# Kernel tuning notes

Measured on AMD Instinct MI355X. Metric: run time of the kernel, lower is better.

## Reference

```python
import jax, jax.numpy as jnp
import numpy as np

# near_sym_a (5,7)-tap biorthogonal analysis filters used by DTCWT level 1
_H0O = np.array([-0.05, 0.25, 0.5, 0.25, -0.05], dtype=np.float32)
_H1O = np.array([-0.0107143, 0.0535714, 0.2607143, -0.6071429,
                 0.2607143, 0.0535714, -0.0107143], dtype=np.float32)

MAGBIAS = np.float32(0.01)


def _filt(x, h, axis):
    """Depthwise 1D correlation of NCHW x along `axis` (2=H rows, 3=W cols)
    with symmetric (half-sample reflect) padding; output same spatial size
    (odd-length filters)."""
    m = h.shape[0] // 2
    pad = [(0, 0)] * 4
    pad[axis] = (m, m)
    xp = jnp.pad(x, pad, mode='symmetric')
    n, c, hh, ww = xp.shape
    k = h.reshape(1, 1, -1, 1) if axis == 2 else h.reshape(1, 1, 1, -1)
    y = jax.lax.conv_general_dilated(
        xp.reshape(n * c, 1, hh, ww), k, (1, 1), 'VALID',
        dimension_numbers=('NCHW', 'OIHW', 'NCHW'))
    return y.reshape(n, c, y.shape[2], y.shape[3])


def _q2c(y):
    # quads -> two complex subimages: ((a-d) + j(b+c), (a+d) + j(b-c)) / sqrt(2)
    y = y * np.float32(1.0 / np.sqrt(2.0))
    a = y[..., 0::2, 0::2]
    b = y[..., 0::2, 1::2]
    c = y[..., 1::2, 0::2]
    d = y[..., 1::2, 1::2]
    return (a - d, b + c), (a + d, b - c)


def _scat_j1(x, h0o, h1o, magbias):
    # level-1 DTCWT: separable biorthogonal filtering (no decimation)
    lo = _filt(x, h0o, 3)   # row lowpass  (along W)
    hi = _filt(x, h1o, 3)   # row highpass
    ll = _filt(lo, h0o, 2)  # (N,C,H,W) lowpass
    lh = _filt(lo, h1o, 2)
    hl = _filt(hi, h0o, 2)
    hh = _filt(hi, h1o, 2)
    # quads -> 6 oriented complex subbands at half resolution
    (d15r, d15i), (d165r, d165i) = _q2c(lh)
    (d45r, d45i), (d135r, d135i) = _q2c(hh)
    (d75r, d75i), (d105r, d105i) = _q2c(hl)
    reals = jnp.stack([d15r, d45r, d75r, d105r, d135r, d165r], axis=1)  # (N,6,C,H/2,W/2)
    imags = jnp.stack([d15i, d45i, d75i, d105i, d135i, d165i], axis=1)
    # smoothed complex magnitude nonlinearity
    r = jnp.sqrt(reals * reals + imags * imags + magbias * magbias) - magbias
    # 2x2 average pool of lowpass
    n, c, hh_, ww_ = ll.shape
    ll = ll.reshape(n, c, hh_ // 2, 2, ww_ // 2, 2).mean(axis=(3, 5))
    b_, _, c_, h_, w_ = r.shape
    r = r.reshape(b_, 6 * c_, h_, w_)
    return ll, r


def setup_inputs() -> dict:
    key = jax.random.key(0)
    x = jax.random.normal(key, (32, 64, 128, 128), dtype=jnp.float32)
    # non-trainable wavelet filter "parameters" (fixed near_sym_a taps)
    return {"x": x, "h0o": jnp.asarray(_H0O), "h1o": jnp.asarray(_H1O)}


def reference(x, h0o, h1o):
    # H, W are even here so the odd-size edge-replication branch is a no-op
    return _scat_j1(x, h0o, h1o, MAGBIAS)
```

## Files before the change

### kernel.cpp

```cpp
#include <hip/hip_runtime.h>
#include <math.h>

#define HALO 3
#define TILE_IN 16
#define LROWS (TILE_IN + 2*HALO)
#define W 128
#define TILE_OUT 8
#define NTILES 8

__device__ __forceinline__ int refl128(int i) {
    i = (i < 0) ? (-1 - i) : i;
    return (i > 127) ? (255 - i) : i;
}

__device__ __forceinline__ float2 vdot7(const float2* A) {
    float2 r;
    r.x = fmaf(-0.0107143f, A[0].x + A[6].x,
          fmaf( 0.0535714f, A[1].x + A[5].x,
          fmaf( 0.2607143f, A[2].x + A[4].x, -0.6071429f * A[3].x)));
    r.y = fmaf(-0.0107143f, A[0].y + A[6].y,
          fmaf( 0.0535714f, A[1].y + A[5].y,
          fmaf( 0.2607143f, A[2].y + A[4].y, -0.6071429f * A[3].y)));
    return r;
}

__device__ __forceinline__ float2 vdot5(const float2* A) {
    float2 r;
    r.x = fmaf(-0.05f, A[0].x + A[4].x, fmaf(0.25f, A[1].x + A[3].x, 0.5f * A[2].x));
    r.y = fmaf(-0.05f, A[0].y + A[4].y, fmaf(0.25f, A[1].y + A[3].y, 0.5f * A[2].y));
    return r;
}

__device__ __forceinline__ float magf(float re, float im) {
    return sqrtf(fmaf(re, re, fmaf(im, im, 1.0e-4f))) - 0.01f;
}

__global__ __launch_bounds__(256) void scat_j1_kernel(
    const float* __restrict__ x,
    float* __restrict__ out_ll,
    float* __restrict__ out_r)
{
    __shared__ float slo[LROWS][W];
    __shared__ float shi[LROWS][W];

    const int raw   = blockIdx.x;
    const int L_id  = (raw & 7) * 2048 + (raw >> 3);
    const int plane = L_id >> 3;
    const int tile  = L_id & 7;
    const int r0    = tile * TILE_IN;
    const int tid   = threadIdx.x;

    const float* __restrict__ xp = x + (size_t)plane * (W * W);

    {
        const int g  = tid & 31;
        const int rb = tid >> 5;
        #pragma unroll
        for (int it = 0; it < 3; ++it) {
            const int lr = it * 8 + rb;
            if (lr < LROWS) {
                const int q = refl128(r0 - HALO + lr);
                const float4* __restrict__ rv = (const float4*)(xp + (size_t)q * W);
                const float4 B = rv[g];
                float4 A = rv[g > 0 ? g - 1 : 0];
                float4 C = rv[g < 31 ? g + 1 : 31];
                const float4 revB = make_float4(B.w, B.z, B.y, B.x);
                if (g == 0)  A = revB;
                if (g == 31) C = revB;
                const float wv[10] = {A.y, A.z, A.w, B.x, B.y, B.z, B.w, C.x, C.y, C.z};
                float4 lo4, hi4;
                float* lop = &lo4.x;
                float* hip_ = &hi4.x;
                #pragma unroll
                for (int j = 0; j < 4; ++j) {
                    const float sA = wv[j]     + wv[j + 6];
                    const float sB = wv[j + 1] + wv[j + 5];
                    const float sC = wv[j + 2] + wv[j + 4];
                    const float ct = wv[j + 3];
                    lop[j]  = fmaf(-0.05f, sB, fmaf(0.25f, sC, 0.5f * ct));
                    hip_[j] = fmaf(-0.0107143f, sA,
                              fmaf( 0.0535714f, sB,
                              fmaf( 0.2607143f, sC, -0.6071429f * ct)));
                }
                ((float4*)&slo[lr][0])[g] = lo4;
                ((float4*)&shi[lr][0])[g] = hi4;
            }
        }
    }
    __syncthreads();

    const int J     = tid & 63;
    const int Ib    = tid >> 6;
    const int c0    = 2 * J;
    const int n     = plane >> 6;
    const int ch    = plane & 63;
    const int Rbase = Ib * 4;
    const float S   = 0.70710678118654752f;

    float2 L[8], H[8];
    #pragma unroll
    for (int t = 0; t < 8; ++t) {
        L[t] = *(const float2*)&slo[Rbase + t][c0];
        H[t] = *(const float2*)&shi[Rbase + t][c0];
    }

    #pragma unroll
    for (int k = 0; k < 2; ++k) {
        const float2 lh_t = vdot7(L);
        const float2 lh_b = vdot7(L + 1);
        const float2 ll_t = vdot5(L + 1);
        const float2 ll_b = vdot5(L + 2);
        const float2 hh_t = vdot7(H);
        const float2 hh_b = vdot7(H + 1);
        const float2 hl_t = vdot5(H + 1);
        const float2 hl_b = vdot5(H + 2);

        float a, b, c_, d;
        a = S * lh_t.x; b = S * lh_t.y; c_ = S * lh_b.x; d = S * lh_b.y;
        const float m15  = magf(a - d, b + c_);
        const float m165 = magf(a + d, b - c_);
        a = S * hh_t.x; b = S * hh_t.y; c_ = S * hh_b.x; d = S * hh_b.y;
        const float m45  = magf(a - d, b + c_);
        const float m135 = magf(a + d, b - c_);
        a = S * hl_t.x; b = S * hl_t.y; c_ = S * hl_b.x; d = S * hl_b.y;
        const float m75  = magf(a - d, b + c_);
        const float m105 = magf(a + d, b - c_);

        const int Il = Ib * 2 + k;
        const int I  = tile * TILE_OUT + Il;

        __builtin_nontemporal_store(
            0.25f * (ll_t.x + ll_t.y + ll_b.x + ll_b.y),
            &out_ll[(size_t)plane * 4096 + I * 64 + J]);

        float* rb_p = out_r + ((size_t)(n * 384 + ch)) * 4096 + (size_t)I * 64 + J;
        __builtin_nontemporal_store(m15,  rb_p + 0u * 262144);
        __builtin_nontemporal_store(m45,  rb_p + 1u * 262144);
        __builtin_nontemporal_store(m75,  rb_p + 2u * 262144);
        __builtin_nontemporal_store(m105, rb_p + 3u * 262144);
        __builtin_nontemporal_store(m135, rb_p + 4u * 262144);
        __builtin_nontemporal_store(m165, rb_p + 5u * 262144);

        if (k == 0) {
            #pragma unroll
            for (int t = 0; t < 6; ++t) { L[t] = L[t + 2]; H[t] = H[t + 2]; }
            const int rn = Rbase + 8;
            L[6] = *(const float2*)&slo[rn][c0];
            L[7] = *(const float2*)&slo[rn + 1][c0];
            H[6] = *(const float2*)&shi[rn][c0];
            H[7] = *(const float2*)&shi[rn + 1][c0];
        }
    }
}

extern "C" void kernel_launch(void* const* d_in, const int* in_sizes, int n_in,
                              void* d_out, int out_size, void* d_ws, size_t ws_size,
                              hipStream_t stream) {
    const float* x = (const float*)d_in[0];
    float* out = (float*)d_out;
    float* out_ll = out;
    float* out_r  = out + 8388608;

    dim3 grid(2048 * NTILES);
    dim3 block(256);
    hipLaunchKernelGGL(scat_j1_kernel, grid, block, 0, stream, x, out_ll, out_r);
}
```

Measured before the change: 77.14 us.

## Process four row tiles per block with register prefetch and double-buffered LDS

```diff
diff --git a/kernel.cpp b/kernel.cpp
--- a/kernel.cpp
+++ b/kernel.cpp
@@ -1,94 +1,84 @@
 #include <hip/hip_runtime.h>
 #include <math.h>
 
-#define HALO 3
+#define W 128
+#define LROWS 22
 #define TILE_IN 16
-#define LROWS (TILE_IN + 2*HALO)
-#define W 128
 #define TILE_OUT 8
-#define NTILES 8
+#define TPB 4
+
+typedef float f2_t __attribute__((ext_vector_type(2)));
 
 __device__ __forceinline__ int refl128(int i) {
     i = (i < 0) ? (-1 - i) : i;
     return (i > 127) ? (255 - i) : i;
 }
 
-__device__ __forceinline__ float2 vdot7(const float2* A) {
-    float2 r;
-    r.x = fmaf(-0.0107143f, A[0].x + A[6].x,
-          fmaf( 0.0535714f, A[1].x + A[5].x,
-          fmaf( 0.2607143f, A[2].x + A[4].x, -0.6071429f * A[3].x)));
-    r.y = fmaf(-0.0107143f, A[0].y + A[6].y,
-          fmaf( 0.0535714f, A[1].y + A[5].y,
-          fmaf( 0.2607143f, A[2].y + A[4].y, -0.6071429f * A[3].y)));
-    return r;
-}
-
-__device__ __forceinline__ float2 vdot5(const float2* A) {
-    float2 r;
-    r.x = fmaf(-0.05f, A[0].x + A[4].x, fmaf(0.25f, A[1].x + A[3].x, 0.5f * A[2].x));
-    r.y = fmaf(-0.05f, A[0].y + A[4].y, fmaf(0.25f, A[1].y + A[3].y, 0.5f * A[2].y));
-    return r;
-}
-
 __device__ __forceinline__ float magf(float re, float im) {
     return sqrtf(fmaf(re, re, fmaf(im, im, 1.0e-4f))) - 0.01f;
 }
 
-__global__ __launch_bounds__(256) void scat_j1_kernel(
-    const float* __restrict__ x,
-    float* __restrict__ out_ll,
-    float* __restrict__ out_r)
-{
-    __shared__ float slo[LROWS][W];
-    __shared__ float shi[LROWS][W];
-
-    const int raw   = blockIdx.x;
-    const int L_id  = (raw & 7) * 2048 + (raw >> 3);
-    const int plane = L_id >> 3;
-    const int tile  = L_id & 7;
-    const int r0    = tile * TILE_IN;
-    const int tid   = threadIdx.x;
-
-    const float* __restrict__ xp = x + (size_t)plane * (W * W);
-
-    {
-        const int g  = tid & 31;
-        const int rb = tid >> 5;
-        #pragma unroll
-        for (int it = 0; it < 3; ++it) {
-            const int lr = it * 8 + rb;
-            if (lr < LROWS) {
-                const int q = refl128(r0 - HALO + lr);
-                const float4* __restrict__ rv = (const float4*)(xp + (size_t)q * W);
-                const float4 B = rv[g];
-                float4 A = rv[g > 0 ? g - 1 : 0];
-                float4 C = rv[g < 31 ? g + 1 : 31];
-                const float4 revB = make_float4(B.w, B.z, B.y, B.x);
-                if (g == 0)  A = revB;
-                if (g == 31) C = revB;
-                const float wv[10] = {A.y, A.z, A.w, B.x, B.y, B.z, B.w, C.x, C.y, C.z};
-                float4 lo4, hi4;
-                float* lop = &lo4.x;
-                float* hip_ = &hi4.x;
-                #pragma unroll
-                for (int j = 0; j < 4; ++j) {
-                    const float sA = wv[j]     + wv[j + 6];
-                    const float sB = wv[j + 1] + wv[j + 5];
-                    const float sC = wv[j + 2] + wv[j + 4];
-                    const float ct = wv[j + 3];
-                    lop[j]  = fmaf(-0.05f, sB, fmaf(0.25f, sC, 0.5f * ct));
-                    hip_[j] = fmaf(-0.0107143f, sA,
-                              fmaf( 0.0535714f, sB,
-                              fmaf( 0.2607143f, sC, -0.6071429f * ct)));
-                }
-                ((float4*)&slo[lr][0])[g] = lo4;
-                ((float4*)&shi[lr][0])[g] = hi4;
+__device__ __forceinline__ void st2(float* p, float a, float b) {
+    f2_t v; v.x = a; v.y = b;
+    __builtin_nontemporal_store(v, (f2_t*)p);
+}
+
+struct Pf { float4 a, b, c; };
+
+__device__ __forceinline__ void pf_tile(const float* __restrict__ xp, int r0,
+                                        int g, int rb, Pf pf[3]) {
+    #pragma unroll
+    for (int it = 0; it < 3; ++it) {
+        const int lr = it * 8 + rb;
+        if (lr < LROWS) {
+            const int q = refl128(r0 - 3 + lr);
+            const float4* __restrict__ rv = (const float4*)(xp + (size_t)q * W);
+            pf[it].b = rv[g];
+            pf[it].a = rv[g > 0 ? g - 1 : 0];
+            pf[it].c = rv[g < 31 ? g + 1 : 31];
+        }
+    }
+}
+
+__device__ __forceinline__ void hwrite(const Pf pf[3], int g, int rb,
+                                       float (* __restrict__ slo)[W],
+                                       float (* __restrict__ shi)[W]) {
+    #pragma unroll
+    for (int it = 0; it < 3; ++it) {
+        const int lr = it * 8 + rb;
+        if (lr < LROWS) {
+            float4 A = pf[it].a;
+            const float4 B = pf[it].b;
+            float4 C = pf[it].c;
+            const float4 revB = make_float4(B.w, B.z, B.y, B.x);
+            if (g == 0)  A = revB;
+            if (g == 31) C = revB;
+            const float wv[10] = {A.y, A.z, A.w, B.x, B.y, B.z, B.w, C.x, C.y, C.z};
+            float4 lo4, hi4;
+            float* lop = &lo4.x;
+            float* hp  = &hi4.x;
+            #pragma unroll
+            for (int j = 0; j < 4; ++j) {
+                const float sA = wv[j]     + wv[j + 6];
+                const float sB = wv[j + 1] + wv[j + 5];
+                const float sC = wv[j + 2] + wv[j + 4];
+                const float ct = wv[j + 3];
+                lop[j] = fmaf(-0.05f, sB, fmaf(0.25f, sC, 0.5f * ct));
+                hp[j]  = fmaf(-0.0107143f, sA,
+                         fmaf( 0.0535714f, sB,
+                         fmaf( 0.2607143f, sC, -0.6071429f * ct)));
             }
-        }
-    }
-    __syncthreads();
-
+            ((float4*)&slo[lr][0])[g] = lo4;
+            ((float4*)&shi[lr][0])[g] = hi4;
+        }
+    }
+}
+
+__device__ __forceinline__ void phase2(const float (* __restrict__ slo)[W],
+                                       const float (* __restrict__ shi)[W],
+                                       int tid, int tile_abs, int plane,
+                                       float* __restrict__ out_ll,
+                                       float* __restrict__ out_r) {
     const int J     = tid & 63;
     const int Ib    = tid >> 6;
     const int c0    = 2 * J;
@@ -106,14 +96,25 @@
 
     #pragma unroll
     for (int k = 0; k < 2; ++k) {
-        const float2 lh_t = vdot7(L);
-        const float2 lh_b = vdot7(L + 1);
-        const float2 ll_t = vdot5(L + 1);
-        const float2 ll_b = vdot5(L + 2);
-        const float2 hh_t = vdot7(H);
-        const float2 hh_b = vdot7(H + 1);
-        const float2 hl_t = vdot5(H + 1);
-        const float2 hl_b = vdot5(H + 2);
+        float2 lh_t, lh_b, ll_t, ll_b, hh_t, hh_b, hl_t, hl_b;
+        {
+            lh_t.x = fmaf(-0.0107143f, L[0].x + L[6].x, fmaf(0.0535714f, L[1].x + L[5].x, fmaf(0.2607143f, L[2].x + L[4].x, -0.6071429f * L[3].x)));
+            lh_t.y = fmaf(-0.0107143f, L[0].y + L[6].y, fmaf(0.0535714f, L[1].y + L[5].y, fmaf(0.2607143f, L[2].y + L[4].y, -0.6071429f * L[3].y)));
+            lh_b.x = fmaf(-0.0107143f, L[1].x + L[7].x, fmaf(0.0535714f, L[2].x + L[6].x, fmaf(0.2607143f, L[3].x + L[5].x, -0.6071429f * L[4].x)));
+            lh_b.y = fmaf(-0.0107143f, L[1].y + L[7].y, fmaf(0.0535714f, L[2].y + L[6].y, fmaf(0.2607143f, L[3].y + L[5].y, -0.6071429f * L[4].y)));
+            ll_t.x = fmaf(-0.05f, L[1].x + L[5].x, fmaf(0.25f, L[2].x + L[4].x, 0.5f * L[3].x));
+            ll_t.y = fmaf(-0.05f, L[1].y + L[5].y, fmaf(0.25f, L[2].y + L[4].y, 0.5f * L[3].y));
+            ll_b.x = fmaf(-0.05f, L[2].x + L[6].x, fmaf(0.25f, L[3].x + L[5].x, 0.5f * L[4].x));
+            ll_b.y = fmaf(-0.05f, L[2].y + L[6].y, fmaf(0.25f, L[3].y + L[5].y, 0.5f * L[4].y));
+            hh_t.x = fmaf(-0.0107143f, H[0].x + H[6].x, fmaf(0.0535714f, H[1].x + H[5].x, fmaf(0.2607143f, H[2].x + H[4].x, -0.6071429f * H[3].x)));
+            hh_t.y = fmaf(-0.0107143f, H[0].y + H[6].y, fmaf(0.0535714f, H[1].y + H[5].y, fmaf(0.2607143f, H[2].y + H[4].y, -0.6071429f * H[3].y)));
+            hh_b.x = fmaf(-0.0107143f, H[1].x + H[7].x, fmaf(0.0535714f, H[2].x + H[6].x, fmaf(0.2607143f, H[3].x + H[5].x, -0.6071429f * H[4].x)));
+            hh_b.y = fmaf(-0.0107143f, H[1].y + H[7].y, fmaf(0.0535714f, H[2].y + H[6].y, fmaf(0.2607143f, H[3].y + H[5].y, -0.6071429f * H[4].y)));
+            hl_t.x = fmaf(-0.05f, H[1].x + H[5].x, fmaf(0.25f, H[2].x + H[4].x, 0.5f * H[3].x));
+            hl_t.y = fmaf(-0.05f, H[1].y + H[5].y, fmaf(0.25f, H[2].y + H[4].y, 0.5f * H[3].y));
+            hl_b.x = fmaf(-0.05f, H[2].x + H[6].x, fmaf(0.25f, H[3].x + H[5].x, 0.5f * H[4].x));
+            hl_b.y = fmaf(-0.05f, H[2].y + H[6].y, fmaf(0.25f, H[3].y + H[5].y, 0.5f * H[4].y));
+        }
 
         float a, b, c_, d;
         a = S * lh_t.x; b = S * lh_t.y; c_ = S * lh_b.x; d = S * lh_b.y;
@@ -127,19 +128,19 @@
         const float m105 = magf(a + d, b - c_);
 
         const int Il = Ib * 2 + k;
-        const int I  = tile * TILE_OUT + Il;
+        const int I  = tile_abs * TILE_OUT + Il;
 
         __builtin_nontemporal_store(
             0.25f * (ll_t.x + ll_t.y + ll_b.x + ll_b.y),
             &out_ll[(size_t)plane * 4096 + I * 64 + J]);
 
-        float* rb_p = out_r + ((size_t)(n * 384 + ch)) * 4096 + (size_t)I * 64 + J;
-        __builtin_nontemporal_store(m15,  rb_p + 0u * 262144);
-        __builtin_nontemporal_store(m45,  rb_p + 1u * 262144);
-        __builtin_nontemporal_store(m75,  rb_p + 2u * 262144);
-        __builtin_nontemporal_store(m105, rb_p + 3u * 262144);
-        __builtin_nontemporal_store(m135, rb_p + 4u * 262144);
-        __builtin_nontemporal_store(m165, rb_p + 5u * 262144);
+        float* rp = out_r + ((size_t)(n * 384 + ch)) * 4096 + (size_t)I * 64 + J;
+        __builtin_nontemporal_store(m15,  rp + 0u * 262144);
+        __builtin_nontemporal_store(m45,  rp + 1u * 262144);
+        __builtin_nontemporal_store(m75,  rp + 2u * 262144);
+        __builtin_nontemporal_store(m105, rp + 3u * 262144);
+        __builtin_nontemporal_store(m135, rp + 4u * 262144);
+        __builtin_nontemporal_store(m165, rp + 5u * 262144);
 
         if (k == 0) {
             #pragma unroll
@@ -153,6 +154,39 @@
     }
 }
 
+__global__ __launch_bounds__(256) void scat_j1_kernel(
+    const float* __restrict__ x,
+    float* __restrict__ out_ll,
+    float* __restrict__ out_r)
+{
+    __shared__ float slo[2][LROWS][W];
+    __shared__ float shi[2][LROWS][W];
+
+    const int raw   = blockIdx.x;
+    const int L_id  = (raw & 7) * 512 + (raw >> 3);
+    const int plane = L_id >> 1;
+    const int half  = L_id & 1;
+    const int tid   = threadIdx.x;
+    const int g     = tid & 31;
+    const int rb    = tid >> 5;
+
+    const float* __restrict__ xp = x + (size_t)plane * (W * W);
+
+    Pf pf[3];
+    pf_tile(xp, (half * TPB) * TILE_IN, g, rb, pf);
+
+    #pragma unroll
+    for (int t = 0; t < TPB; ++t) {
+        const int tile_abs = half * TPB + t;
+        const int buf = t & 1;
+        hwrite(pf, g, rb, slo[buf], shi[buf]);
+        __syncthreads();
+        if (t + 1 < TPB)
+            pf_tile(xp, (tile_abs + 1) * TILE_IN, g, rb, pf);
+        phase2(slo[buf], shi[buf], tid, tile_abs, plane, out_ll, out_r);
+    }
+}
+
 extern "C" void kernel_launch(void* const* d_in, const int* in_sizes, int n_in,
                               void* d_out, int out_size, void* d_ws, size_t ws_size,
                               hipStream_t stream) {
@@ -161,7 +195,7 @@
     float* out_ll = out;
     float* out_r  = out + 8388608;
 
-    dim3 grid(2048 * NTILES);
+    dim3 grid(4096);
     dim3 block(256);
     hipLaunchKernelGGL(scat_j1_kernel, grid, block, 0, stream, x, out_ll, out_r);
 }
```

Result: slower. 89.02 us (+15.4%).

## Remap column pass so each thread computes two output columns with float4 LDS reads

Applied to the files above, without the earlier changes.

```diff
diff --git a/kernel.cpp b/kernel.cpp
--- a/kernel.cpp
+++ b/kernel.cpp
@@ -1,38 +1,37 @@
 #include <hip/hip_runtime.h>
 #include <math.h>
 
-#define HALO 3
+#define W 128
+#define LROWS 22
 #define TILE_IN 16
-#define LROWS (TILE_IN + 2*HALO)
-#define W 128
 #define TILE_OUT 8
 #define NTILES 8
+
+typedef float f2_t __attribute__((ext_vector_type(2)));
 
 __device__ __forceinline__ int refl128(int i) {
     i = (i < 0) ? (-1 - i) : i;
     return (i > 127) ? (255 - i) : i;
 }
 
-__device__ __forceinline__ float2 vdot7(const float2* A) {
-    float2 r;
-    r.x = fmaf(-0.0107143f, A[0].x + A[6].x,
-          fmaf( 0.0535714f, A[1].x + A[5].x,
-          fmaf( 0.2607143f, A[2].x + A[4].x, -0.6071429f * A[3].x)));
-    r.y = fmaf(-0.0107143f, A[0].y + A[6].y,
-          fmaf( 0.0535714f, A[1].y + A[5].y,
-          fmaf( 0.2607143f, A[2].y + A[4].y, -0.6071429f * A[3].y)));
-    return r;
+__device__ __forceinline__ float magf(float re, float im) {
+    return sqrtf(fmaf(re, re, fmaf(im, im, 1.0e-4f))) - 0.01f;
 }
 
-__device__ __forceinline__ float2 vdot5(const float2* A) {
-    float2 r;
-    r.x = fmaf(-0.05f, A[0].x + A[4].x, fmaf(0.25f, A[1].x + A[3].x, 0.5f * A[2].x));
-    r.y = fmaf(-0.05f, A[0].y + A[4].y, fmaf(0.25f, A[1].y + A[3].y, 0.5f * A[2].y));
-    return r;
+__device__ __forceinline__ void st2(float* p, float a, float b) {
+    f2_t v; v.x = a; v.y = b;
+    __builtin_nontemporal_store(v, (f2_t*)p);
 }
 
-__device__ __forceinline__ float magf(float re, float im) {
-    return sqrtf(fmaf(re, re, fmaf(im, im, 1.0e-4f))) - 0.01f;
+__device__ __forceinline__ float4 add4(float4 a, float4 b) {
+    return make_float4(a.x + b.x, a.y + b.y, a.z + b.z, a.w + b.w);
+}
+__device__ __forceinline__ float4 mul4(float k, float4 a) {
+    return make_float4(k * a.x, k * a.y, k * a.z, k * a.w);
+}
+__device__ __forceinline__ float4 fma4(float k, float4 a, float4 acc) {
+    return make_float4(fmaf(k, a.x, acc.x), fmaf(k, a.y, acc.y),
+                       fmaf(k, a.z, acc.z), fmaf(k, a.w, acc.w));
 }
 
 __global__ __launch_bounds__(256) void scat_j1_kernel(
@@ -59,7 +58,7 @@
         for (int it = 0; it < 3; ++it) {
             const int lr = it * 8 + rb;
             if (lr < LROWS) {
-                const int q = refl128(r0 - HALO + lr);
+                const int q = refl128(r0 - 3 + lr);
                 const float4* __restrict__ rv = (const float4*)(xp + (size_t)q * W);
                 const float4 B = rv[g];
                 float4 A = rv[g > 0 ? g - 1 : 0];
@@ -70,17 +69,17 @@
                 const float wv[10] = {A.y, A.z, A.w, B.x, B.y, B.z, B.w, C.x, C.y, C.z};
                 float4 lo4, hi4;
                 float* lop = &lo4.x;
-                float* hip_ = &hi4.x;
+                float* hp  = &hi4.x;
                 #pragma unroll
                 for (int j = 0; j < 4; ++j) {
                     const float sA = wv[j]     + wv[j + 6];
                     const float sB = wv[j + 1] + wv[j + 5];
                     const float sC = wv[j + 2] + wv[j + 4];
                     const float ct = wv[j + 3];
-                    lop[j]  = fmaf(-0.05f, sB, fmaf(0.25f, sC, 0.5f * ct));
-                    hip_[j] = fmaf(-0.0107143f, sA,
-                              fmaf( 0.0535714f, sB,
-                              fmaf( 0.2607143f, sC, -0.6071429f * ct)));
+                    lop[j] = fmaf(-0.05f, sB, fmaf(0.25f, sC, 0.5f * ct));
+                    hp[j]  = fmaf(-0.0107143f, sA,
+                             fmaf( 0.0535714f, sB,
+                             fmaf( 0.2607143f, sC, -0.6071429f * ct)));
                 }
                 ((float4*)&slo[lr][0])[g] = lo4;
                 ((float4*)&shi[lr][0])[g] = hi4;
@@ -89,68 +88,71 @@
     }
     __syncthreads();
 
-    const int J     = tid & 63;
-    const int Ib    = tid >> 6;
-    const int c0    = 2 * J;
-    const int n     = plane >> 6;
-    const int ch    = plane & 63;
-    const int Rbase = Ib * 4;
+    const int cp = tid & 31;
+    const int Ib = tid >> 5;
+    const int R0 = 2 * Ib;
+    const int n  = plane >> 6;
+    const int ch = plane & 63;
+
     const float S   = 0.70710678118654752f;
+    const float a7  = -0.0107143f * S, b7c = 0.0535714f * S,
+                c7  =  0.2607143f * S, d7c = -0.6071429f * S;
+    const float a5s = -0.05f * S, b5s = 0.25f * S, c5s = 0.5f * S;
+    const float p5a = -0.0125f, p5b = 0.0625f, p5c = 0.125f;
 
-    float2 L[8], H[8];
-    #pragma unroll
-    for (int t = 0; t < 8; ++t) {
-        L[t] = *(const float2*)&slo[Rbase + t][c0];
-        H[t] = *(const float2*)&shi[Rbase + t][c0];
+    float m15_0, m15_1, m165_0, m165_1, ll0, ll1;
+    {
+        float4 v[8];
+        #pragma unroll
+        for (int t = 0; t < 8; ++t) v[t] = ((const float4*)&slo[R0 + t][0])[cp];
+        const float4 s06 = add4(v[0], v[6]), s15 = add4(v[1], v[5]),
+                     s24 = add4(v[2], v[4]), s17 = add4(v[1], v[7]),
+                     s26 = add4(v[2], v[6]), s35 = add4(v[3], v[5]);
+        const float4 t7 = fma4(a7, s06, fma4(b7c, s15, fma4(c7, s24, mul4(d7c, v[3]))));
+        const float4 bo = fma4(a7, s17, fma4(b7c, s26, fma4(c7, s35, mul4(d7c, v[4]))));
+        const float4 lt = fma4(p5a, s15, fma4(p5b, s24, mul4(p5c, v[3])));
+        const float4 lb = fma4(p5a, s26, fma4(p5b, s35, mul4(p5c, v[4])));
+        m15_0  = magf(t7.x - bo.y, t7.y + bo.x);
+        m15_1  = magf(t7.z - bo.w, t7.w + bo.z);
+        m165_0 = magf(t7.x + bo.y, t7.y - bo.x);
+        m165_1 = magf(t7.z + bo.w, t7.w - bo.z);
+        ll0 = (lt.x + lt.y) + (lb.x + lb.y);
+        ll1 = (lt.z + lt.w) + (lb.z + lb.w);
+    }
+    float m45_0, m45_1, m135_0, m135_1, m75_0, m75_1, m105_0, m105_1;
+    {
+        float4 v[8];
+        #pragma unroll
+        for (int t = 0; t < 8; ++t) v[t] = ((const float4*)&shi[R0 + t][0])[cp];
+        const float4 s06 = add4(v[0], v[6]), s15 = add4(v[1], v[5]),
+                     s24 = add4(v[2], v[4]), s17 = add4(v[1], v[7]),
+                     s26 = add4(v[2], v[6]), s35 = add4(v[3], v[5]);
+        const float4 t7 = fma4(a7, s06, fma4(b7c, s15, fma4(c7, s24, mul4(d7c, v[3]))));
+        const float4 bo = fma4(a7, s17, fma4(b7c, s26, fma4(c7, s35, mul4(d7c, v[4]))));
+        const float4 ht = fma4(a5s, s15, fma4(b5s, s24, mul4(c5s, v[3])));
+        const float4 hb = fma4(a5s, s26, fma4(b5s, s35, mul4(c5s, v[4])));
+        m45_0  = magf(t7.x - bo.y, t7.y + bo.x);
+        m45_1  = magf(t7.z - bo.w, t7.w + bo.z);
+        m135_0 = magf(t7.x + bo.y, t7.y - bo.x);
+        m135_1 = magf(t7.z + bo.w, t7.w - bo.z);
+        m75_0  = magf(ht.x - hb.y, ht.y + hb.x);
+        m75_1  = magf(ht.z - hb.w, ht.w + hb.z);
+        m105_0 = magf(ht.x + hb.y, ht.y - hb.x);
+        m105_1 = magf(ht.z + hb.w, ht.w - hb.z);
     }
 
-    #pragma unroll
-    for (int k = 0; k < 2; ++k) {
-        const float2 lh_t = vdot7(L);
-        const float2 lh_b = vdot7(L + 1);
-        const float2 ll_t = vdot5(L + 1);
-        const float2 ll_b = vdot5(L + 2);
-        const float2 hh_t = vdot7(H);
-        const float2 hh_b = vdot7(H + 1);
-        const float2 hl_t = vdot5(H + 1);
-        const float2 hl_b = vdot5(H + 2);
+    const int I  = tile * TILE_OUT + Ib;
+    const int J0 = 2 * cp;
 
-        float a, b, c_, d;
-        a = S * lh_t.x; b = S * lh_t.y; c_ = S * lh_b.x; d = S * lh_b.y;
-        const float m15  = magf(a - d, b + c_);
-        const float m165 = magf(a + d, b - c_);
-        a = S * hh_t.x; b = S * hh_t.y; c_ = S * hh_b.x; d = S * hh_b.y;
-        const float m45  = magf(a - d, b + c_);
-        const float m135 = magf(a + d, b - c_);
-        a = S * hl_t.x; b = S * hl_t.y; c_ = S * hl_b.x; d = S * hl_b.y;
-        const float m75  = magf(a - d, b + c_);
-        const float m105 = magf(a + d, b - c_);
+    st2(out_ll + (size_t)plane * 4096 + (size_t)I * 64 + J0, ll0, ll1);
 
-        const int Il = Ib * 2 + k;
-        const int I  = tile * TILE_OUT + Il;
-
-        __builtin_nontemporal_store(
-            0.25f * (ll_t.x + ll_t.y + ll_b.x + ll_b.y),
-            &out_ll[(size_t)plane * 4096 + I * 64 + J]);
-
-        float* rb_p = out_r + ((size_t)(n * 384 + ch)) * 4096 + (size_t)I * 64 + J;
-        __builtin_nontemporal_store(m15,  rb_p + 0u * 262144);
-        __builtin_nontemporal_store(m45,  rb_p + 1u * 262144);
-        __builtin_nontemporal_store(m75,  rb_p + 2u * 262144);
-        __builtin_nontemporal_store(m105, rb_p + 3u * 262144);
-        __builtin_nontemporal_store(m135, rb_p + 4u * 262144);
-        __builtin_nontemporal_store(m165, rb_p + 5u * 262144);
-
-        if (k == 0) {
-            #pragma unroll
-            for (int t = 0; t < 6; ++t) { L[t] = L[t + 2]; H[t] = H[t + 2]; }
-            const int rn = Rbase + 8;
-            L[6] = *(const float2*)&slo[rn][c0];
-            L[7] = *(const float2*)&slo[rn + 1][c0];
-            H[6] = *(const float2*)&shi[rn][c0];
-            H[7] = *(const float2*)&shi[rn + 1][c0];
-        }
-    }
+    float* rp = out_r + ((size_t)(n * 384 + ch)) * 4096 + (size_t)I * 64 + J0;
+    st2(rp + 0u * 262144u, m15_0,  m15_1);
+    st2(rp + 1u * 262144u, m45_0,  m45_1);
+    st2(rp + 2u * 262144u, m75_0,  m75_1);
+    st2(rp + 3u * 262144u, m105_0, m105_1);
+    st2(rp + 4u * 262144u, m135_0, m135_1);
+    st2(rp + 5u * 262144u, m165_0, m165_1);
 }
 
 extern "C" void kernel_launch(void* const* d_in, const int* in_sizes, int n_in,
```

Measured after the change: 80.48 us. 4.3% more time.
